# Kernel tuning notes

Hardware: AMD Instinct MI355X
Metric: run time of the kernel (lower is better)

## Reference

```python
import jax, jax.numpy as jnp
import numpy as np

B, S, H = 32, 64, 768        # batch, weeks (seq len), hidden / encoding width
TPW = 32                     # avg encodings per (batch, week) segment
ZD, CD = 32, 16              # noise dim, condition dim
NL, OUT, HOR = 2, 1, 24      # lstm layers, output size, horizon
TOT = B * S * TPW            # total ragged encoding rows = 65536
NSEG = B * S                 # number of segments = 2048
IN = ZD + CD + H             # lstm input size = 816


def setup_inputs() -> dict:
    key = jax.random.key(0)
    ks = jax.random.split(key, 18)
    s_h = 1.0 / np.sqrt(H)
    s_in = 1.0 / np.sqrt(IN)
    inp = {
        "z": jax.random.normal(ks[0], (B, S, ZD), jnp.float32),
        "cond": jax.random.normal(ks[1], (B, S, CD), jnp.float32),
        "encs": jax.random.normal(ks[2], (TOT, H), jnp.float32),
        # equal-size segments (32 rows per week); math is identical for ragged ids
        "segment_ids": (jnp.arange(TOT) // TPW).astype(jnp.int32),
        # filter: two stacked Linear(768,768), no activation (as in source)
        "W1": jax.random.normal(ks[3], (H, H), jnp.float32) * s_h,
        "b1": jnp.zeros((H,), jnp.float32),
        "W2": jax.random.normal(ks[4], (H, H), jnp.float32) * s_h,
        "b2": jnp.zeros((H,), jnp.float32),
        # LSTM layer 0 (input IN -> H), PyTorch gate order i,f,g,o
        "Wih0": jax.random.normal(ks[5], (4 * H, IN), jnp.float32) * s_in,
        "Whh0": jax.random.normal(ks[6], (4 * H, H), jnp.float32) * s_h,
        "bih0": jnp.zeros((4 * H,), jnp.float32),
        "bhh0": jnp.zeros((4 * H,), jnp.float32),
        # LSTM layer 1 (H -> H)
        "Wih1": jax.random.normal(ks[7], (4 * H, H), jnp.float32) * s_h,
        "Whh1": jax.random.normal(ks[8], (4 * H, H), jnp.float32) * s_h,
        "bih1": jnp.zeros((4 * H,), jnp.float32),
        "bhh1": jnp.zeros((4 * H,), jnp.float32),
        # output Linear(H, OUT)
        "Wout": jax.random.normal(ks[9], (OUT, H), jnp.float32) * s_h,
        "bout": jnp.zeros((OUT,), jnp.float32),
    }
    return inp


def _lstm_layer(x, Wih, Whh, bih, bhh):
    # x: [B, S, in] -> outputs [B, S, H]; zero initial state as in the module
    Hh = Whh.shape[1]
    xg = jnp.einsum("bsi,gi->sbg", x, Wih) + (bih + bhh)  # precompute input gates

    def step(carry, xt):
        h, c = carry
        g = xt + h @ Whh.T
        i, f, gg, o = jnp.split(g, 4, axis=-1)
        c = jax.nn.sigmoid(f) * c + jax.nn.sigmoid(i) * jnp.tanh(gg)
        h = jax.nn.sigmoid(o) * jnp.tanh(c)
        return (h, c), h

    h0 = jnp.zeros((x.shape[0], Hh), x.dtype)
    _, hs = jax.lax.scan(step, (h0, h0), xg)
    return jnp.transpose(hs, (1, 0, 2))  # [B, S, H]


def reference(z, cond, encs, segment_ids, W1, b1, W2, b2,
              Wih0, Whh0, bih0, bhh0, Wih1, Whh1, bih1, bhh1, Wout, bout):
    # per-row 2-layer linear filter (fused over all batches/weeks)
    filt = (encs @ W1.T + b1) @ W2.T + b2  # [TOT, H]
    # segment mean per (batch, week)
    seg_sum = jax.ops.segment_sum(filt, segment_ids, num_segments=NSEG)
    cnt = jax.ops.segment_sum(jnp.ones((TOT, 1), filt.dtype), segment_ids,
                              num_segments=NSEG)
    encoded = (seg_sum / jnp.maximum(cnt, 1.0)).reshape(B, S, H)
    # concat noise, condition, pooled encodings -> 2-layer LSTM -> linear head
    x = jnp.concatenate([z, cond, encoded], axis=-1)  # [B, S, IN]
    h = _lstm_layer(x, Wih0, Whh0, bih0, bhh0)
    h = _lstm_layer(h, Wih1, Whh1, bih1, bhh1)
    preds = h @ Wout.T + bout  # [B, S, OUT]
    return preds[:, :HOR, :], encoded
```

## Files before the change

kernel.cpp:

```cpp
#include <hip/hip_runtime.h>
#include <cstddef>

#define NB 32
#define NS 64
#define NH 768
#define NSEG_ (NB*NS)
#define NIN 816
#define G4 3072
#define HOR_ 24
#define FBLK 192
#define LTHR 512

typedef __attribute__((ext_vector_type(8))) short bf16x8;
typedef __attribute__((ext_vector_type(4))) float f32x4;
typedef __attribute__((ext_vector_type(8))) unsigned short u16x8;

#define HP2 776
#define SMEM_BYTES (2*32*HP2*2 + 8*528*4)

#define OFF_X      0
#define SZ_X       (NSEG_*NIN)
#define OFF_MEAN   (OFF_X + SZ_X)
#define SZ_MEAN    (NSEG_*NH)
#define OFF_TMP    (OFF_MEAN + SZ_MEAN)
#define OFF_H0PK   (OFF_TMP + SZ_MEAN)
#define OFF_H1PK   (OFF_H0PK + SZ_MEAN)
#define OFF_XG     (OFF_H1PK + SZ_MEAN)
#define SZ_XG      (NSEG_*G4)
#define OFF_HZERO  (OFF_XG + SZ_XG)
#define SZ_HZERO   (NB*NH)
#define OFF_FLG    (OFF_HZERO + SZ_HZERO)

__device__ __forceinline__ void coh_store_u16(unsigned short* p, unsigned short v) {
  __hip_atomic_store(p, v, __ATOMIC_RELAXED, __HIP_MEMORY_SCOPE_AGENT);
}

__device__ __forceinline__ void split_bf16(float v, unsigned short& hi,
                                           unsigned short& lo) {
  const unsigned u = __float_as_uint(v);
  const unsigned r = u + 0x7FFFu + ((u >> 16) & 1u);
  hi = (unsigned short)(r >> 16);
  const float rem = v - __uint_as_float((r >> 16) << 16);
  lo = (unsigned short)(__float_as_uint(rem) >> 16);
}

__device__ __forceinline__ unsigned short rne_bf16(float v) {
  const unsigned u = __float_as_uint(v);
  return (unsigned short)((u + 0x7FFFu + ((u >> 16) & 1u)) >> 16);
}

__device__ __forceinline__ void stage_hi(const unsigned short* __restrict__ src,
                                         unsigned short* plane, int sb, int sch) {
  #pragma unroll
  for (int it = 0; it < 6; ++it) {
    const int k0 = (sch + it * 16) * 8;
    uint4 v = *(const uint4*)(src + (size_t)sb * NH + k0);
    *(uint4*)(&plane[sb * HP2 + k0]) = v;
  }
}

__global__ __launch_bounds__(192) void seg_mean_kernel(
    const float* __restrict__ encs, float* __restrict__ mean) {
  const int s = blockIdx.x;
  const int t = threadIdx.x;
  const float4* base = (const float4*)(encs + (size_t)s * 32 * NH);
  float4 a = {0.f, 0.f, 0.f, 0.f};
  #pragma unroll 4
  for (int r = 0; r < 32; ++r) {
    float4 v = base[(size_t)r * (NH / 4) + t];
    a.x += v.x; a.y += v.y; a.z += v.z; a.w += v.w;
  }
  const float inv = 1.f / 32.f;
  float4 o = {a.x * inv, a.y * inv, a.z * inv, a.w * inv};
  ((float4*)mean)[(size_t)s * (NH / 4) + t] = o;
}

__global__ __launch_bounds__(256) void gemm_mfma_nt(
    const float* __restrict__ A, const float* __restrict__ W,
    const float* __restrict__ bias1, const float* __restrict__ bias2,
    float* __restrict__ C, int M, int N, int K) {
  __shared__ unsigned short Ahi[64 * 40];
  __shared__ unsigned short Alo[64 * 40];
  __shared__ unsigned short Whi[64 * 40];
  __shared__ unsigned short Wlo[64 * 40];
  const int tid = threadIdx.x;
  const int bm = blockIdx.y, bn = blockIdx.x;
  const int lane = tid & 63;
  const int wid  = tid >> 6;
  const int lm = lane & 15;
  const int lk = lane >> 4;
  const int srow = tid >> 2;
  const int skc  = (tid & 3) * 8;

  const float* Ap = A + (size_t)(bm * 64 + srow) * K;
  const float* Wp = W + (size_t)(bn * 64 + srow) * K;

  f32x4 acc[4];
  #pragma unroll
  for (int nf = 0; nf < 4; ++nf) acc[nf] = (f32x4){0.f, 0.f, 0.f, 0.f};

  for (int k0 = 0; k0 < K; k0 += 32) {
    float va[8], vw[8];
    if (k0 + skc + 8 <= K) {
      float4 a0 = *(const float4*)(Ap + k0 + skc);
      float4 a1 = *(const float4*)(Ap + k0 + skc + 4);
      float4 w0 = *(const float4*)(Wp + k0 + skc);
      float4 w1 = *(const float4*)(Wp + k0 + skc + 4);
      va[0]=a0.x; va[1]=a0.y; va[2]=a0.z; va[3]=a0.w;
      va[4]=a1.x; va[5]=a1.y; va[6]=a1.z; va[7]=a1.w;
      vw[0]=w0.x; vw[1]=w0.y; vw[2]=w0.z; vw[3]=w0.w;
      vw[4]=w1.x; vw[5]=w1.y; vw[6]=w1.z; vw[7]=w1.w;
    } else {
      #pragma unroll
      for (int i = 0; i < 8; ++i) { va[i] = 0.f; vw[i] = 0.f; }
    }
    u16x8 AH, AL, WH, WL;
    #pragma unroll
    for (int i = 0; i < 8; ++i) {
      unsigned short h, l;
      split_bf16(va[i], h, l); AH[i] = h; AL[i] = l;
      split_bf16(vw[i], h, l); WH[i] = h; WL[i] = l;
    }
    __syncthreads();
    *(u16x8*)(&Ahi[srow * 40 + skc]) = AH;
    *(u16x8*)(&Alo[srow * 40 + skc]) = AL;
    *(u16x8*)(&Whi[srow * 40 + skc]) = WH;
    *(u16x8*)(&Wlo[srow * 40 + skc]) = WL;
    __syncthreads();
    bf16x8 ah = *(bf16x8*)(&Ahi[(wid * 16 + lm) * 40 + lk * 8]);
    bf16x8 al = *(bf16x8*)(&Alo[(wid * 16 + lm) * 40 + lk * 8]);
    #pragma unroll
    for (int nf = 0; nf < 4; ++nf) {
      bf16x8 bh = *(bf16x8*)(&Whi[(nf * 16 + lm) * 40 + lk * 8]);
      bf16x8 bl = *(bf16x8*)(&Wlo[(nf * 16 + lm) * 40 + lk * 8]);
      acc[nf] = __builtin_amdgcn_mfma_f32_16x16x32_bf16(ah, bh, acc[nf], 0, 0, 0);
      acc[nf] = __builtin_amdgcn_mfma_f32_16x16x32_bf16(ah, bl, acc[nf], 0, 0, 0);
      acc[nf] = __builtin_amdgcn_mfma_f32_16x16x32_bf16(al, bh, acc[nf], 0, 0, 0);
    }
  }
  #pragma unroll
  for (int nf = 0; nf < 4; ++nf) {
    const int gn = bn * 64 + nf * 16 + lm;
    float bb = 0.f;
    if (bias1) bb += bias1[gn];
    if (bias2) bb += bias2[gn];
    #pragma unroll
    for (int r4 = 0; r4 < 4; ++r4) {
      const int gm = bm * 64 + wid * 16 + lk * 4 + r4;
      C[(size_t)gm * N + gn] = acc[nf][r4] + bb;
    }
  }
}

__global__ __launch_bounds__(256) void build_x_kernel(
    const float* __restrict__ z, const float* __restrict__ cond,
    const float* __restrict__ enc, float* __restrict__ x) {
  const int idx = blockIdx.x * 256 + threadIdx.x;
  const int r = idx / NIN, c = idx % NIN;
  const int s = r >> 5, b = r & 31;
  const int bs = b * NS + s;
  float v;
  if (c < 32)      v = z[bs * 32 + c];
  else if (c < 48) v = cond[bs * 16 + (c - 32)];
  else             v = enc[(size_t)bs * NH + (c - 48)];
  x[idx] = v;
}

__global__ __launch_bounds__(LTHR)
__attribute__((amdgpu_waves_per_eu(2, 2)))
void lstm_merged(
    const float* __restrict__ xg0,
    const float* __restrict__ Whh0,
    const float* __restrict__ Wih1,
    const float* __restrict__ Whh1,
    const float* __restrict__ bih1,
    const float* __restrict__ bhh1,
    const unsigned short* __restrict__ hzero,
    unsigned short* h0,
    unsigned short* h1,
    unsigned* flags) {
  extern __shared__ __align__(16) unsigned short smem_us[];
  unsigned short* pA  = smem_us;
  unsigned short* pB  = smem_us + 32 * HP2;
  float*          gsp = (float*)(smem_us + 2 * 32 * HP2);

  const int tid  = threadIdx.x;
  const int lane = tid & 63;
  const int wid  = tid >> 6;
  const bool wL1 = (wid >= 4);
  const int kh   = wid & 3;
  const int lm   = lane & 15;
  const int lk   = lane >> 4;
  const int lblk = blockIdx.x;

  const int grow = (lm >> 2) * NH + lblk * 4 + (lm & 3);
  const float* WhhP = wL1 ? Whh1 : Whh0;
  bf16x8 whi[6], wlo[6];
  #pragma unroll
  for (int s6 = 0; s6 < 6; ++s6) {
    const float* wp = WhhP + (size_t)grow * NH + kh * 192 + s6 * 32 + lk * 8;
    float4 a = *(const float4*)wp;
    float4 b = *(const float4*)(wp + 4);
    float vv[8] = {a.x, a.y, a.z, a.w, b.x, b.y, b.z, b.w};
    #pragma unroll
    for (int i = 0; i < 8; ++i) {
      unsigned short h, l;
      split_bf16(vv[i], h, l);
      whi[s6][i] = (short)h;
      wlo[s6][i] = (short)l;
    }
  }

  const int jp = tid >> 5;
  const int bp = tid & 31;
  const bool pwL1 = (jp >= 4);
  const int jloc = jp & 3;
  float c_reg = 0.f;
  float bi = 0.f, bf_ = 0.f, bg = 0.f, bo = 0.f;
  if (tid < 256 && pwL1) {
    const int jj = lblk * 4 + jloc;
    bi  = bih1[0 * NH + jj] + bhh1[0 * NH + jj];
    bf_ = bih1[1 * NH + jj] + bhh1[1 * NH + jj];
    bg  = bih1[2 * NH + jj] + bhh1[2 * NH + jj];
    bo  = bih1[3 * NH + jj] + bhh1[3 * NH + jj];
  }
  const int sb  = tid >> 4;
  const int sch = tid & 15;

  for (int e = 0; e <= NS; ++e) {
    const unsigned short* h0r = (e == 0) ? hzero : h0 + (size_t)(e - 1) * NB * NH;
    const unsigned short* h1r = (e <= 1) ? hzero : h1 + (size_t)(e - 2) * NB * NH;
    float xgv0 = 0.f, xgv1 = 0.f, xgv2 = 0.f, xgv3 = 0.f;
    if (tid < 256 && !pwL1 && e < NS) {
      const float* xr = xg0 + (size_t)(e * NB + bp) * G4 + (lblk * 4 + jloc);
      xgv0 = xr[0]; xgv1 = xr[NH]; xgv2 = xr[2 * NH]; xgv3 = xr[3 * NH];
    }
    stage_hi(h0r, pA, sb, sch);
    stage_hi(h1r, pB, sb, sch);
    __syncthreads();
    f32x4 acc0 = {0.f, 0.f, 0.f, 0.f};
    f32x4 acc1 = {0.f, 0.f, 0.f, 0.f};
    if (!wL1) {
      #pragma unroll
      for (int s6 = 0; s6 < 6; ++s6) {
        const int kb = kh * 192 + s6 * 32 + lk * 8;
        bf16x8 b0 = *(bf16x8*)(&pA[lm * HP2 + kb]);
        bf16x8 b1 = *(bf16x8*)(&pA[(16 + lm) * HP2 + kb]);
        acc0 = __builtin_amdgcn_mfma_f32_16x16x32_bf16(whi[s6], b0, acc0, 0, 0, 0);
        acc0 = __builtin_amdgcn_mfma_f32_16x16x32_bf16(wlo[s6], b0, acc0, 0, 0, 0);
        acc1 = __builtin_amdgcn_mfma_f32_16x16x32_bf16(whi[s6], b1, acc1, 0, 0, 0);
        acc1 = __builtin_amdgcn_mfma_f32_16x16x32_bf16(wlo[s6], b1, acc1, 0, 0, 0);
      }
    } else {
      #pragma unroll
      for (int s6 = 0; s6 < 6; ++s6) {
        const float* up = Wih1 + (size_t)grow * NH + kh * 192 + s6 * 32 + lk * 8;
        float4 ua = *(const float4*)up;
        float4 ub = *(const float4*)(up + 4);
        float uv[8] = {ua.x, ua.y, ua.z, ua.w, ub.x, ub.y, ub.z, ub.w};
        bf16x8 uh, ul;
        #pragma unroll
        for (int i = 0; i < 8; ++i) {
          unsigned short h, l;
          split_bf16(uv[i], h, l);
          uh[i] = (short)h;
          ul[i] = (short)l;
        }
        const int kb = kh * 192 + s6 * 32 + lk * 8;
        bf16x8 b0 = *(bf16x8*)(&pA[lm * HP2 + kb]);
        bf16x8 b1 = *(bf16x8*)(&pA[(16 + lm) * HP2 + kb]);
        acc0 = __builtin_amdgcn_mfma_f32_16x16x32_bf16(uh, b0, acc0, 0, 0, 0);
        acc0 = __builtin_amdgcn_mfma_f32_16x16x32_bf16(ul, b0, acc0, 0, 0, 0);
        acc1 = __builtin_amdgcn_mfma_f32_16x16x32_bf16(uh, b1, acc1, 0, 0, 0);
        acc1 = __builtin_amdgcn_mfma_f32_16x16x32_bf16(ul, b1, acc1, 0, 0, 0);
      }
      #pragma unroll
      for (int s6 = 0; s6 < 6; ++s6) {
        const int kb = kh * 192 + s6 * 32 + lk * 8;
        bf16x8 b0 = *(bf16x8*)(&pB[lm * HP2 + kb]);
        bf16x8 b1 = *(bf16x8*)(&pB[(16 + lm) * HP2 + kb]);
        acc0 = __builtin_amdgcn_mfma_f32_16x16x32_bf16(whi[s6], b0, acc0, 0, 0, 0);
        acc0 = __builtin_amdgcn_mfma_f32_16x16x32_bf16(wlo[s6], b0, acc0, 0, 0, 0);
        acc1 = __builtin_amdgcn_mfma_f32_16x16x32_bf16(whi[s6], b1, acc1, 0, 0, 0);
        acc1 = __builtin_amdgcn_mfma_f32_16x16x32_bf16(wlo[s6], b1, acc1, 0, 0, 0);
      }
    }
    #pragma unroll
    for (int r4 = 0; r4 < 4; ++r4) {
      gsp[wid * 528 + (lk * 4 + r4) * 33 + lm]      = acc0[r4];
      gsp[wid * 528 + (lk * 4 + r4) * 33 + 16 + lm] = acc1[r4];
    }
    __syncthreads();
    if (tid < 256) {
      if (!pwL1) {
        if (e < NS) {
          float sum[4];
          #pragma unroll
          for (int g = 0; g < 4; ++g) {
            const int row = g * 4 + jloc;
            sum[g] = gsp[0 * 528 + row * 33 + bp] + gsp[1 * 528 + row * 33 + bp] +
                     gsp[2 * 528 + row * 33 + bp] + gsp[3 * 528 + row * 33 + bp];
          }
          const float si = 1.f / (1.f + expf(-(sum[0] + xgv0)));
          const float sf = 1.f / (1.f + expf(-(sum[1] + xgv1)));
          const float so = 1.f / (1.f + expf(-(sum[3] + xgv3)));
          c_reg = sf * c_reg + si * tanhf(sum[2] + xgv2);
          const float hnew = so * tanhf(c_reg);
          coh_store_u16(&h0[(size_t)(e * NB + bp) * NH + lblk * 4 + jloc],
                        rne_bf16(hnew));
        }
      } else {
        if (e >= 1) {
          const int t = e - 1;
          float sum[4];
          #pragma unroll
          for (int g = 0; g < 4; ++g) {
            const int row = g * 4 + jloc;
            sum[g] = gsp[4 * 528 + row * 33 + bp] + gsp[5 * 528 + row * 33 + bp] +
                     gsp[6 * 528 + row * 33 + bp] + gsp[7 * 528 + row * 33 + bp];
          }
          const float si = 1.f / (1.f + expf(-(sum[0] + bi)));
          const float sf = 1.f / (1.f + expf(-(sum[1] + bf_)));
          const float so = 1.f / (1.f + expf(-(sum[3] + bo)));
          c_reg = sf * c_reg + si * tanhf(sum[2] + bg);
          const float hnew = so * tanhf(c_reg);
          coh_store_u16(&h1[(size_t)(t * NB + bp) * NH + lblk * 4 + jloc],
                        rne_bf16(hnew));
        }
      }
    }
    if (e < NS) {
      __syncthreads();
      if (tid == 0) {
        asm volatile("s_waitcnt vmcnt(0)" ::: "memory");
        __hip_atomic_store(&flags[(unsigned)blockIdx.x * 4], (unsigned)(e + 1),
                           __ATOMIC_RELAXED, __HIP_MEMORY_SCOPE_AGENT);
      }
      if (tid < FBLK) {
        while (__hip_atomic_load(&flags[(unsigned)tid * 4], __ATOMIC_RELAXED,
                                 __HIP_MEMORY_SCOPE_AGENT) < (unsigned)(e + 1))
          __builtin_amdgcn_s_sleep(1);
      }
      __syncthreads();
    }
  }
}

__global__ __launch_bounds__(64) void head_kernel(
    const unsigned short* __restrict__ h1, const float* __restrict__ Wout,
    const float* __restrict__ bout, float* __restrict__ preds) {
  const int o = blockIdx.x;
  const int b = o / HOR_, s = o % HOR_;
  const int l = threadIdx.x;
  const unsigned short* h = h1 + (size_t)(s * NB + b) * NH;
  float acc = 0.f;
  #pragma unroll
  for (int k = l; k < NH; k += 64) {
    const float v = __uint_as_float(((unsigned)h[k]) << 16);
    acc += v * Wout[k];
  }
  #pragma unroll
  for (int m = 32; m; m >>= 1) acc += __shfl_xor(acc, m);
  if (l == 0) preds[o] = acc + bout[0];
}

extern "C" void kernel_launch(void* const* d_in, const int* in_sizes, int n_in,
                              void* d_out, int out_size, void* d_ws, size_t ws_size,
                              hipStream_t stream) {
  const float* z    = (const float*)d_in[0];
  const float* cond = (const float*)d_in[1];
  const float* encs = (const float*)d_in[2];
  const float* W1   = (const float*)d_in[4];
  const float* b1   = (const float*)d_in[5];
  const float* W2   = (const float*)d_in[6];
  const float* b2   = (const float*)d_in[7];
  const float* Wih0 = (const float*)d_in[8];
  const float* Whh0 = (const float*)d_in[9];
  const float* bih0 = (const float*)d_in[10];
  const float* bhh0 = (const float*)d_in[11];
  const float* Wih1 = (const float*)d_in[12];
  const float* Whh1 = (const float*)d_in[13];
  const float* bih1 = (const float*)d_in[14];
  const float* bhh1 = (const float*)d_in[15];
  const float* Wout = (const float*)d_in[16];
  const float* bout = (const float*)d_in[17];

  float* out     = (float*)d_out;
  float* preds   = out;
  float* enc_out = out + NB * HOR_;

  float* ws    = (float*)d_ws;
  float* xb    = ws + OFF_X;
  float* mean  = ws + OFF_MEAN;
  float* tmp   = ws + OFF_TMP;
  unsigned short* h0 = (unsigned short*)(ws + OFF_H0PK);
  unsigned short* h1 = (unsigned short*)(ws + OFF_H1PK);
  float* xg    = ws + OFF_XG;
  unsigned short* hzero = (unsigned short*)(ws + OFF_HZERO);
  unsigned* flags = (unsigned*)(ws + OFF_FLG);

  (void)hipFuncSetAttribute(reinterpret_cast<const void*>(lstm_merged),
                            hipFuncAttributeMaxDynamicSharedMemorySize,
                            160 * 1024);

  seg_mean_kernel<<<NSEG_, 192, 0, stream>>>(encs, mean);
  gemm_mfma_nt<<<dim3(NH / 64, NSEG_ / 64), 256, 0, stream>>>(
      mean, W1, b1, nullptr, tmp, NSEG_, NH, NH);
  gemm_mfma_nt<<<dim3(NH / 64, NSEG_ / 64), 256, 0, stream>>>(
      tmp, W2, b2, nullptr, enc_out, NSEG_, NH, NH);
  build_x_kernel<<<(NSEG_ * NIN) / 256, 256, 0, stream>>>(z, cond, enc_out, xb);
  gemm_mfma_nt<<<dim3(G4 / 64, NSEG_ / 64), 256, 0, stream>>>(
      xb, Wih0, bih0, bhh0, xg, NSEG_, G4, NIN);
  hipMemsetAsync(hzero, 0, (size_t)(SZ_HZERO + 1024) * sizeof(float), stream);
  lstm_merged<<<FBLK, LTHR, SMEM_BYTES, stream>>>(
      xg, Whh0, Wih1, Whh1, bih1, bhh1, hzero, h0, h1, flags);
  head_kernel<<<NB * HOR_, 64, 0, stream>>>(h1, Wout, bout, preds);
}
```

Before: 582.5 us.

## Pre-split operands to packed bf16 hi/lo and use 128x128 tile GEMM

The layer-0 input-projection GEMM now works on pre-split operands. A new kernel packs Wih0 into interleaved bf16 hi/lo words, and the concat kernel emits packed x directly. A new 512-thread GEMM with 128x128 tiles then reads those fragments from shared memory, so the float-to-bf16 split no longer happens inside the inner loop and more data is reused per tile. The cost is an extra weight-packing pass on every call, and the packed weights reuse the mean/tmp workspace, which are no longer needed at that point.

```diff
diff --git a/kernel.cpp b/kernel.cpp
--- a/kernel.cpp
+++ b/kernel.cpp
@@ -30,6 +30,7 @@
 #define OFF_HZERO  (OFF_XG + SZ_XG)
 #define SZ_HZERO   (NB*NH)
 #define OFF_FLG    (OFF_HZERO + SZ_HZERO)
+#define OFF_WPK    OFF_MEAN
 
 __device__ __forceinline__ void coh_store_u16(unsigned short* p, unsigned short v) {
   __hip_atomic_store(p, v, __ATOMIC_RELAXED, __HIP_MEMORY_SCOPE_AGENT);
@@ -47,6 +48,24 @@
 __device__ __forceinline__ unsigned short rne_bf16(float v) {
   const unsigned u = __float_as_uint(v);
   return (unsigned short)((u + 0x7FFFu + ((u >> 16) & 1u)) >> 16);
+}
+
+__device__ __forceinline__ unsigned pack_hilo(float v) {
+  unsigned short h, l;
+  split_bf16(v, h, l);
+  return ((unsigned)h << 16) | l;
+}
+
+__device__ __forceinline__ void read_frag(const unsigned* __restrict__ plane,
+                                          int idx, bf16x8& hi, bf16x8& lo) {
+  const uint4 w0 = *(const uint4*)(plane + idx);
+  const uint4 w1 = *(const uint4*)(plane + idx + 4);
+  const unsigned ww[8] = {w0.x, w0.y, w0.z, w0.w, w1.x, w1.y, w1.z, w1.w};
+  #pragma unroll
+  for (int i = 0; i < 8; ++i) {
+    hi[i] = (short)(ww[i] >> 16);
+    lo[i] = (short)(ww[i] & 0xffffu);
+  }
 }
 
 __device__ __forceinline__ void stage_hi(const unsigned short* __restrict__ src,
@@ -152,9 +171,20 @@
   }
 }
 
-__global__ __launch_bounds__(256) void build_x_kernel(
+__global__ __launch_bounds__(256) void pack_w_kernel(
+    const float* __restrict__ src, unsigned* __restrict__ dst, int n4) {
+  const int i = blockIdx.x * 256 + threadIdx.x;
+  if (i >= n4) return;
+  float4 v = ((const float4*)src)[i];
+  uint4 o;
+  o.x = pack_hilo(v.x); o.y = pack_hilo(v.y);
+  o.z = pack_hilo(v.z); o.w = pack_hilo(v.w);
+  ((uint4*)dst)[i] = o;
+}
+
+__global__ __launch_bounds__(256) void build_x_pk_kernel(
     const float* __restrict__ z, const float* __restrict__ cond,
-    const float* __restrict__ enc, float* __restrict__ x) {
+    const float* __restrict__ enc, unsigned* __restrict__ x) {
   const int idx = blockIdx.x * 256 + threadIdx.x;
   const int r = idx / NIN, c = idx % NIN;
   const int s = r >> 5, b = r & 31;
@@ -163,7 +193,69 @@
   if (c < 32)      v = z[bs * 32 + c];
   else if (c < 48) v = cond[bs * 16 + (c - 32)];
   else             v = enc[(size_t)bs * NH + (c - 48)];
-  x[idx] = v;
+  x[idx] = pack_hilo(v);
+}
+
+__global__ __launch_bounds__(512) void gemm_pk128(
+    const unsigned* __restrict__ A, const unsigned* __restrict__ W,
+    const float* __restrict__ bias1, const float* __restrict__ bias2,
+    float* __restrict__ C, int M, int N, int K) {
+  __shared__ unsigned As[128 * 36];
+  __shared__ unsigned Ws[128 * 36];
+  const int tid = threadIdx.x;
+  const int bm = blockIdx.y, bn = blockIdx.x;
+  const int lane = tid & 63;
+  const int wid  = tid >> 6;
+  const int lm = lane & 15;
+  const int lk = lane >> 4;
+  const int st   = tid & 255;
+  const int srow = st >> 1;
+  const int sc0  = (st & 1) * 4;
+  const unsigned* gsrc = (tid < 256)
+      ? A + (size_t)(bm * 128 + srow) * K
+      : W + (size_t)(bn * 128 + srow) * K;
+  unsigned* ldst = (tid < 256) ? As : Ws;
+
+  f32x4 acc[8];
+  #pragma unroll
+  for (int nf = 0; nf < 8; ++nf) acc[nf] = (f32x4){0.f, 0.f, 0.f, 0.f};
+
+  for (int k0 = 0; k0 < K; k0 += 32) {
+    uint4 v[4];
+    #pragma unroll
+    for (int q = 0; q < 4; ++q) {
+      const int kc = k0 + (sc0 + q) * 4;
+      if (kc + 4 <= K) v[q] = *(const uint4*)(gsrc + kc);
+      else             v[q] = (uint4){0u, 0u, 0u, 0u};
+    }
+    __syncthreads();
+    #pragma unroll
+    for (int q = 0; q < 4; ++q)
+      *(uint4*)(&ldst[srow * 36 + (sc0 + q) * 4]) = v[q];
+    __syncthreads();
+    bf16x8 ah, al;
+    read_frag(As, (wid * 16 + lm) * 36 + lk * 8, ah, al);
+    #pragma unroll
+    for (int nf = 0; nf < 8; ++nf) {
+      bf16x8 bh, bl;
+      read_frag(Ws, (nf * 16 + lm) * 36 + lk * 8, bh, bl);
+      acc[nf] = __builtin_amdgcn_mfma_f32_16x16x32_bf16(ah, bh, acc[nf], 0, 0, 0);
+      acc[nf] = __builtin_amdgcn_mfma_f32_16x16x32_bf16(ah, bl, acc[nf], 0, 0, 0);
+      acc[nf] = __builtin_amdgcn_mfma_f32_16x16x32_bf16(al, bh, acc[nf], 0, 0, 0);
+    }
+  }
+  #pragma unroll
+  for (int nf = 0; nf < 8; ++nf) {
+    const int gn = bn * 128 + nf * 16 + lm;
+    float bb = 0.f;
+    if (bias1) bb += bias1[gn];
+    if (bias2) bb += bias2[gn];
+    #pragma unroll
+    for (int r4 = 0; r4 < 4; ++r4) {
+      const int gm = bm * 128 + wid * 16 + lk * 4 + r4;
+      C[(size_t)gm * N + gn] = acc[nf][r4] + bb;
+    }
+  }
 }
 
 __global__ __launch_bounds__(LTHR)
@@ -390,9 +482,10 @@
   float* enc_out = out + NB * HOR_;
 
   float* ws    = (float*)d_ws;
-  float* xb    = ws + OFF_X;
+  unsigned* xbpk = (unsigned*)(ws + OFF_X);
   float* mean  = ws + OFF_MEAN;
   float* tmp   = ws + OFF_TMP;
+  unsigned* wpk  = (unsigned*)(ws + OFF_WPK);
   unsigned short* h0 = (unsigned short*)(ws + OFF_H0PK);
   unsigned short* h1 = (unsigned short*)(ws + OFF_H1PK);
   float* xg    = ws + OFF_XG;
@@ -408,9 +501,12 @@
       mean, W1, b1, nullptr, tmp, NSEG_, NH, NH);
   gemm_mfma_nt<<<dim3(NH / 64, NSEG_ / 64), 256, 0, stream>>>(
       tmp, W2, b2, nullptr, enc_out, NSEG_, NH, NH);
-  build_x_kernel<<<(NSEG_ * NIN) / 256, 256, 0, stream>>>(z, cond, enc_out, xb);
-  gemm_mfma_nt<<<dim3(G4 / 64, NSEG_ / 64), 256, 0, stream>>>(
-      xb, Wih0, bih0, bhh0, xg, NSEG_, G4, NIN);
+  pack_w_kernel<<<(G4 * NIN / 4 + 255) / 256, 256, 0, stream>>>(
+      Wih0, wpk, G4 * NIN / 4);
+  build_x_pk_kernel<<<(NSEG_ * NIN) / 256, 256, 0, stream>>>(
+      z, cond, enc_out, xbpk);
+  gemm_pk128<<<dim3(G4 / 128, NSEG_ / 128), 512, 0, stream>>>(
+      xbpk, wpk, bih0, bhh0, xg, NSEG_, G4, NIN);
   hipMemsetAsync(hzero, 0, (size_t)(SZ_HZERO + 1024) * sizeof(float), stream);
   lstm_merged<<<FBLK, LTHR, SMEM_BYTES, stream>>>(
       xg, Whh0, Wih1, Whh1, bih1, bhh1, hzero, h0, h1, flags);
```

Measured after the change: 590.3 us. No clear change (+1.3%).

## Fold two linear filter layers into one matrix and prepack Wih1 as bf16 hi/lo

Applied to the files above, without the earlier changes.

The two stacked linear filters are folded into a single combined weight W2·W1 with a combined bias, computed per call through a transpose, a small GEMM and a bias kernel. This replaces the second 2048x768x768 GEMM with a 768x768x768 one. Separately, Wih1 is pre-split into packed bf16 hi/lo pairs once per call, so the LSTM's layer-1 waves no longer redo the fp32 split on every timestep. The cost is a few extra small kernel launches, slightly different rounding from the folded product, and the packed weights reusing the mean buffer region, which is dead once the filter GEMM has run.

```diff
diff --git a/kernel.cpp b/kernel.cpp
--- a/kernel.cpp
+++ b/kernel.cpp
@@ -30,6 +30,10 @@
 #define OFF_HZERO  (OFF_XG + SZ_XG)
 #define SZ_HZERO   (NB*NH)
 #define OFF_FLG    (OFF_HZERO + SZ_HZERO)
+#define OFF_W1T    OFF_TMP
+#define OFF_W12    (OFF_TMP + 620000)
+#define OFF_B12    (OFF_TMP + 1250000)
+#define OFF_WPK    OFF_MEAN
 
 __device__ __forceinline__ void coh_store_u16(unsigned short* p, unsigned short v) {
   __hip_atomic_store(p, v, __ATOMIC_RELAXED, __HIP_MEMORY_SCOPE_AGENT);
@@ -47,6 +51,22 @@
 __device__ __forceinline__ unsigned short rne_bf16(float v) {
   const unsigned u = __float_as_uint(v);
   return (unsigned short)((u + 0x7FFFu + ((u >> 16) & 1u)) >> 16);
+}
+
+__device__ __forceinline__ unsigned pack_hilo(float v) {
+  unsigned short h, l;
+  split_bf16(v, h, l);
+  return ((unsigned)h << 16) | l;
+}
+
+__device__ __forceinline__ void unpack8(const uint4& a, const uint4& b,
+                                        bf16x8& hi, bf16x8& lo) {
+  const unsigned ww[8] = {a.x, a.y, a.z, a.w, b.x, b.y, b.z, b.w};
+  #pragma unroll
+  for (int i = 0; i < 8; ++i) {
+    hi[i] = (short)(ww[i] >> 16);
+    lo[i] = (short)(ww[i] & 0xffffu);
+  }
 }
 
 __device__ __forceinline__ void stage_hi(const unsigned short* __restrict__ src,
@@ -73,6 +93,31 @@
   const float inv = 1.f / 32.f;
   float4 o = {a.x * inv, a.y * inv, a.z * inv, a.w * inv};
   ((float4*)mean)[(size_t)s * (NH / 4) + t] = o;
+}
+
+__global__ __launch_bounds__(256) void transpose_kernel(
+    const float* __restrict__ src, float* __restrict__ dst, int n) {
+  __shared__ float tile[32][33];
+  const int nt = n / 32;
+  const int bx = blockIdx.x % nt, by = blockIdx.x / nt;
+  const int tx = threadIdx.x & 31, ty = threadIdx.x >> 5;
+  #pragma unroll
+  for (int i = 0; i < 32; i += 8)
+    tile[ty + i][tx] = src[(size_t)(by * 32 + ty + i) * n + bx * 32 + tx];
+  __syncthreads();
+  #pragma unroll
+  for (int i = 0; i < 32; i += 8)
+    dst[(size_t)(bx * 32 + ty + i) * n + by * 32 + tx] = tile[tx][ty + i];
+}
+
+__global__ __launch_bounds__(256) void b12_kernel(
+    const float* __restrict__ W2, const float* __restrict__ b1,
+    const float* __restrict__ b2, float* __restrict__ b12) {
+  const int i = blockIdx.x * 256 + threadIdx.x;
+  if (i >= NH) return;
+  float acc = b2[i];
+  for (int k = 0; k < NH; ++k) acc += W2[(size_t)i * NH + k] * b1[k];
+  b12[i] = acc;
 }
 
 __global__ __launch_bounds__(256) void gemm_mfma_nt(
@@ -152,6 +197,17 @@
   }
 }
 
+__global__ __launch_bounds__(256) void pack_w_kernel(
+    const float* __restrict__ src, unsigned* __restrict__ dst, int n4) {
+  const int i = blockIdx.x * 256 + threadIdx.x;
+  if (i >= n4) return;
+  float4 v = ((const float4*)src)[i];
+  uint4 o;
+  o.x = pack_hilo(v.x); o.y = pack_hilo(v.y);
+  o.z = pack_hilo(v.z); o.w = pack_hilo(v.w);
+  ((uint4*)dst)[i] = o;
+}
+
 __global__ __launch_bounds__(256) void build_x_kernel(
     const float* __restrict__ z, const float* __restrict__ cond,
     const float* __restrict__ enc, float* __restrict__ x) {
@@ -171,7 +227,7 @@
 void lstm_merged(
     const float* __restrict__ xg0,
     const float* __restrict__ Whh0,
-    const float* __restrict__ Wih1,
+    const unsigned* __restrict__ Wih1pk,
     const float* __restrict__ Whh1,
     const float* __restrict__ bih1,
     const float* __restrict__ bhh1,
@@ -254,18 +310,11 @@
     } else {
       #pragma unroll
       for (int s6 = 0; s6 < 6; ++s6) {
-        const float* up = Wih1 + (size_t)grow * NH + kh * 192 + s6 * 32 + lk * 8;
-        float4 ua = *(const float4*)up;
-        float4 ub = *(const float4*)(up + 4);
-        float uv[8] = {ua.x, ua.y, ua.z, ua.w, ub.x, ub.y, ub.z, ub.w};
+        const unsigned* up = Wih1pk + (size_t)grow * NH + kh * 192 + s6 * 32 + lk * 8;
+        uint4 ua = *(const uint4*)up;
+        uint4 ub = *(const uint4*)(up + 4);
         bf16x8 uh, ul;
-        #pragma unroll
-        for (int i = 0; i < 8; ++i) {
-          unsigned short h, l;
-          split_bf16(uv[i], h, l);
-          uh[i] = (short)h;
-          ul[i] = (short)l;
-        }
+        unpack8(ua, ub, uh, ul);
         const int kb = kh * 192 + s6 * 32 + lk * 8;
         bf16x8 b0 = *(bf16x8*)(&pA[lm * HP2 + kb]);
         bf16x8 b1 = *(bf16x8*)(&pA[(16 + lm) * HP2 + kb]);
@@ -392,7 +441,10 @@
   float* ws    = (float*)d_ws;
   float* xb    = ws + OFF_X;
   float* mean  = ws + OFF_MEAN;
-  float* tmp   = ws + OFF_TMP;
+  float* w1t   = ws + OFF_W1T;
+  float* w12   = ws + OFF_W12;
+  float* b12   = ws + OFF_B12;
+  unsigned* wih1pk = (unsigned*)(ws + OFF_WPK);
   unsigned short* h0 = (unsigned short*)(ws + OFF_H0PK);
   unsigned short* h1 = (unsigned short*)(ws + OFF_H1PK);
   float* xg    = ws + OFF_XG;
@@ -404,15 +456,19 @@
                             160 * 1024);
 
   seg_mean_kernel<<<NSEG_, 192, 0, stream>>>(encs, mean);
+  transpose_kernel<<<(NH / 32) * (NH / 32), 256, 0, stream>>>(W1, w1t, NH);
+  gemm_mfma_nt<<<dim3(NH / 64, NH / 64), 256, 0, stream>>>(
+      W2, w1t, nullptr, nullptr, w12, NH, NH, NH);
+  b12_kernel<<<(NH + 255) / 256, 256, 0, stream>>>(W2, b1, b2, b12);
   gemm_mfma_nt<<<dim3(NH / 64, NSEG_ / 64), 256, 0, stream>>>(
-      mean, W1, b1, nullptr, tmp, NSEG_, NH, NH);
-  gemm_mfma_nt<<<dim3(NH / 64, NSEG_ / 64), 256, 0, stream>>>(
-      tmp, W2, b2, nullptr, enc_out, NSEG_, NH, NH);
+      mean, w12, b12, nullptr, enc_out, NSEG_, NH, NH);
   build_x_kernel<<<(NSEG_ * NIN) / 256, 256, 0, stream>>>(z, cond, enc_out, xb);
+  pack_w_kernel<<<(G4 * NH / 4 + 255) / 256, 256, 0, stream>>>(
+      Wih1, wih1pk, G4 * NH / 4);
   gemm_mfma_nt<<<dim3(G4 / 64, NSEG_ / 64), 256, 0, stream>>>(
       xb, Wih0, bih0, bhh0, xg, NSEG_, G4, NIN);
   hipMemsetAsync(hzero, 0, (size_t)(SZ_HZERO + 1024) * sizeof(float), stream);
   lstm_merged<<<FBLK, LTHR, SMEM_BYTES, stream>>>(
-      xg, Whh0, Wih1, Whh1, bih1, bhh1, hzero, h0, h1, flags);
+      xg, Whh0, wih1pk, Whh1, bih1, bhh1, hzero, h0, h1, flags);
   head_kernel<<<NB * HOR_, 64, 0, stream>>>(h1, Wout, bout, preds);
 }
```

Result: slower. 595.6 us (+2.2%).
